# Optimization experiments

Measured on AMD Instinct MI355X. Metric: run time of the kernel, lower is better.

Reference implementation:

```python
import jax, jax.numpy as jnp
import numpy as np

# Module constants from CheckboxDetector.__init__ / _postprocess
N = 8192            # candidate detections
C = 2               # checkbox classes (checked / unchecked)
THR = 0.7           # confidence threshold (self.threshold)
IOU_THR = 0.5       # torchvision.ops.nms iou_threshold
INPUT_H, INPUT_W = 1280.0, 1280.0   # self.input_shape
IMG_H, IMG_W = 2480.0, 3508.0       # original image (A4 @ 300dpi)
SCALER = max(IMG_W / INPUT_W, IMG_H / INPUT_H)
EPS = 1e-9


def setup_inputs() -> dict:
    key = jax.random.key(0)
    k1, k2, k3 = jax.random.split(key, 3)
    cls_conf = jax.random.uniform(k1, (N, C), dtype=jnp.float32)
    # well-formed xyxy boxes inside the 1280x1280 canvas
    xy = jax.random.uniform(k2, (N, 2), dtype=jnp.float32, minval=0.0, maxval=1200.0)
    wh = jax.random.uniform(k3, (N, 2), dtype=jnp.float32, minval=8.0, maxval=80.0)
    bboxes = jnp.concatenate([xy, xy + wh], axis=1)  # [N,4]
    return {"cls_conf": cls_conf, "bboxes": bboxes}


def _pairwise_iou(boxes):
    # boxes: [N,4] xyxy -> iou: [N,N]
    x1, y1, x2, y2 = boxes[:, 0], boxes[:, 1], boxes[:, 2], boxes[:, 3]
    area = (x2 - x1) * (y2 - y1)
    iw = jnp.clip(jnp.minimum(x2[:, None], x2[None, :]) - jnp.maximum(x1[:, None], x1[None, :]), 0.0)
    ih = jnp.clip(jnp.minimum(y2[:, None], y2[None, :]) - jnp.maximum(y1[:, None], y1[None, :]), 0.0)
    inter = iw * ih
    return inter / (area[:, None] + area[None, :] - inter + EPS)


def reference(cls_conf, bboxes):
    # _threshold: keep rows with any class confidence > THR (mask instead of
    # dynamic filtering, for fixed shapes under jit)
    valid = jnp.any(cls_conf > THR, axis=1)            # [N]
    scores = jnp.max(cls_conf, axis=1)                 # cls_conf.max(1)
    masked_scores = jnp.where(valid, scores, -jnp.inf)

    # _nms: sort by score desc, greedy IoU suppression (torchvision semantics)
    order = jnp.argsort(-masked_scores)
    b = bboxes[order]          # [N,4]
    c = cls_conf[order]        # [N,C]
    v = valid[order]           # [N]

    iou = _pairwise_iou(b)     # [N,N]  (256 MB: memory-bound core)
    idx = jnp.arange(N)

    def body(i, keep):
        # box i (if still kept & valid) suppresses later boxes overlapping > IOU_THR
        sup = (iou[i] > IOU_THR) & (idx > i) & keep[i]
        return keep & ~sup

    keep = jax.lax.fori_loop(0, N, body, v)            # [N] bool

    # _postprocess tail: rescale boxes to original image size; suppressed
    # detections are zeroed (mask semantics in place of dynamic gather).
    kf = keep.astype(cls_conf.dtype)[:, None]
    boxes_out = b * SCALER * kf                        # [N,4]
    conf_out = c * kf                                  # [N,C]
    return jnp.concatenate([boxes_out, conf_out], axis=1)  # [N, 4+C]
```

## Files before the change

### kernel.cpp

```cpp
#include <hip/hip_runtime.h>
#include <math.h>

#define N_BOX 8192
#define NW 128
#define NTHR 512
#define LCAP 24576
#define NPB 512
#define TPW 4
#define RPT 4
#define NRB 128
#define WPB 8
#define NWAVE (NPB * WPB)
#define SLOT 128
#define WSPT (NWAVE / NTHR)
#define NCH 8
#define THR_C 0.7f
#define IOU_THR_C 0.5f
#define EPS_C 1e-9f

__device__ __constant__ float kScaler = (float)(3508.0 / 1280.0);

static __device__ __forceinline__ unsigned long long key_from(float c0, float c1, int i) {
    bool valid = (c0 > THR_C) || (c1 > THR_C);
    float ms = valid ? fmaxf(c0, c1) : -INFINITY;
    unsigned int u = __float_as_uint(ms);
    unsigned int m = (u & 0x80000000u) ? ~u : (u | 0x80000000u);
    unsigned int d = ~m;
    return ((unsigned long long)d << 32) | (unsigned int)i;
}

__global__ __launch_bounds__(NTHR) void stageA(const float* __restrict__ conf,
                                               const float* __restrict__ bboxes,
                                               int* __restrict__ partial,
                                               unsigned int* __restrict__ wcnt,
                                               unsigned int* __restrict__ wslot) {
    int b = blockIdx.x;
    int t = threadIdx.x;
    if (b < NPB) {
        int w = b >> 2;
        int h = b & (TPW - 1);
        int ntiles = (w >> 5) + 1;
        int waveid = b * WPB + (t >> 6);
        int lane = t & 63;
        if (h >= ntiles) {
            if (lane == 0) wcnt[waveid] = 0u;
            return;
        }
        __shared__ float4 cb[64];
        __shared__ float carea[64];
        __shared__ unsigned long long cbk[64];
        __shared__ unsigned long long jvS;
        if (t < 64) {
            int j = (w << 6) + t;
            float4 c = ((const float4*)bboxes)[j];
            cb[t] = c;
            carea[t] = (c.z - c.x) * (c.w - c.y);
            float2 cc = ((const float2*)conf)[j];
            cbk[t] = key_from(cc.x, cc.y, j);
            unsigned long long bv = __ballot((cc.x > THR_C) || (cc.y > THR_C));
            if (t == 0) jvS = bv;
        }
        __syncthreads();
        unsigned long long jv = jvS;
        int ibase = h << 11;
        float4 rb_[RPT];
        float ra_[RPT];
        unsigned long long ki_[RPT], jm_[RPT];
#pragma unroll
        for (int q = 0; q < RPT; ++q) {
            int i = ibase + (q << 9) + t;
            int rel = i - (w << 6);
            unsigned long long jm = jv;
            if (rel >= 63) jm = 0ull;
            else if (rel >= 0) jm &= ~((2ull << rel) - 1ull);
            float2 cc = ((const float2*)conf)[i];
            if (!((cc.x > THR_C) || (cc.y > THR_C))) jm = 0ull;
            jm_[q] = jm;
            float4 r = ((const float4*)bboxes)[i];
            rb_[q] = r;
            ra_[q] = (r.z - r.x) * (r.w - r.y);
            ki_[q] = key_from(cc.x, cc.y, i);
        }
        int wc = 0;
        bool wave_has = __any((jm_[0] | jm_[1] | jm_[2] | jm_[3]) != 0ull);
        if (wave_has) {
            unsigned long long bits[RPT] = {0ull, 0ull, 0ull, 0ull};
            for (int bb = 0; bb < 64; ++bb) {
                float4 c = cb[bb];
                float ca = carea[bb];
#pragma unroll
                for (int q = 0; q < RPT; ++q) {
                    float iw = fminf(rb_[q].z, c.z) - fmaxf(rb_[q].x, c.x);
                    float ih = fminf(rb_[q].w, c.w) - fmaxf(rb_[q].y, c.y);
                    iw = fmaxf(iw, 0.0f);
                    ih = fmaxf(ih, 0.0f);
                    float inter = iw * ih;
                    float sab = ra_[q] + ca;
                    if (inter > 0.2f * sab) {
                        float iou = inter / (ra_[q] + ca - inter + EPS_C);
                        if (iou > IOU_THR_C) bits[q] |= (1ull << bb);
                    }
                }
            }
#pragma unroll
            for (int q = 0; q < RPT; ++q) {
                unsigned long long eb = bits[q] & jm_[q];
                if (__any(eb != 0ull)) {
                    int ec = __popcll(eb);
                    int pre = ec;
#pragma unroll
                    for (int d = 1; d < 64; d <<= 1) {
                        int vv = __shfl_up(pre, d, 64);
                        if (lane >= d) pre += vv;
                    }
                    int tot = __shfl(pre, 63, 64);
                    int idx = wc + pre - ec;
                    unsigned long long tb = eb;
                    int i = ibase + (q << 9) + t;
                    while (tb) {
                        int bb = __builtin_ctzll(tb); tb &= tb - 1;
                        if (idx < SLOT) {
                            int j = (w << 6) + bb;
                            unsigned int e = (ki_[q] < cbk[bb])
                                             ? (((unsigned int)i << 13) | (unsigned int)j)
                                             : (((unsigned int)j << 13) | (unsigned int)i);
                            wslot[(size_t)waveid * SLOT + idx] = e;
                        }
                        ++idx;
                    }
                    wc += tot;
                }
            }
        }
        if (lane == 0) wcnt[waveid] = (unsigned int)wc;
    } else {
        __shared__ unsigned long long ck[1024];
        int rb = b - NPB;
        int ech = rb >> 3;
        int cch = rb & 7;
        for (int l = t; l < 1024; l += NTHR) {
            int j = (cch << 10) + l;
            float2 cc = ((const float2*)conf)[j];
            ck[l] = key_from(cc.x, cc.y, j);
        }
        __syncthreads();
        int i = (ech << 9) + t;
        float2 ci = ((const float2*)conf)[i];
        unsigned long long ki = key_from(ci.x, ci.y, i);
        const ulonglong2* ckp = (const ulonglong2*)ck;
        int a0 = 0, a1 = 0, a2 = 0, a3 = 0;
#pragma unroll 4
        for (int l = 0; l < 512; l += 2) {
            ulonglong2 u = ckp[l];
            ulonglong2 v = ckp[l + 1];
            a0 += (u.x < ki) ? 1 : 0;
            a1 += (u.y < ki) ? 1 : 0;
            a2 += (v.x < ki) ? 1 : 0;
            a3 += (v.y < ki) ? 1 : 0;
        }
        partial[cch * N_BOX + i] = (a0 + a1) + (a2 + a3);
    }
}

__global__ __launch_bounds__(NTHR) void stageB(const float* __restrict__ conf,
                                               const float* __restrict__ bboxes,
                                               const int* __restrict__ partial,
                                               const unsigned int* __restrict__ wcnt,
                                               const unsigned int* __restrict__ wslot,
                                               float* __restrict__ out) {
    __shared__ unsigned int eL[LCAP];
    __shared__ unsigned long long kL[NW], tL[NW], vL[NW];
    __shared__ int wsum[NTHR];
    __shared__ int chg[3];
    __shared__ int fbF, nvF;
    int t = threadIdx.x;
    if (t == 0) { fbF = 0; nvF = 0; chg[0] = 0; chg[1] = 0; chg[2] = 0; }
    for (int base = 0; base < N_BOX; base += NTHR) {
        int i = base + t;
        float2 cc = ((const float2*)conf)[i];
        unsigned long long bv = __ballot((cc.x > THR_C) || (cc.y > THR_C));
        if ((t & 63) == 0) vL[i >> 6] = bv;
    }
    int nq[WSPT], myo[WSPT];
    int s = 0;
    bool ov = false;
#pragma unroll
    for (int q = 0; q < WSPT; ++q) {
        int v = (int)wcnt[t * WSPT + q];
        nq[q] = v; myo[q] = s; s += v;
        if (v > SLOT) ov = true;
    }
    wsum[t] = s;
    __syncthreads();
    if (t < NW) kL[t] = vL[t];
    for (int off = 1; off < NTHR; off <<= 1) {
        int v = (t >= off) ? wsum[t - off] : 0;
        __syncthreads();
        wsum[t] += v;
        __syncthreads();
    }
    int ebase = wsum[t] - s;
    int totE = wsum[NTHR - 1];
    if (ov || totE > LCAP) fbF = 1;
    __syncthreads();
    int fb = fbF;
    if (!fb) {
#pragma unroll
        for (int q = 0; q < WSPT; ++q) {
            int w2 = t * WSPT + q;
            int off = ebase + myo[q];
            for (int k = 0; k < nq[q]; ++k)
                eL[off + k] = wslot[(size_t)w2 * SLOT + k];
        }
    }
    __syncthreads();
    if (!fb) {
        for (int it = 0; it < N_BOX; ++it) {
            if (t < NW) tL[t] = 0ull;
            __syncthreads();
            for (int e = t; e < totE; e += NTHR) {
                unsigned int ed = eL[e];
                int src = (int)(ed >> 13);
                if ((kL[src >> 6] >> (src & 63)) & 1ull) {
                    int tg = (int)(ed & 8191u);
                    atomicOr(&tL[tg >> 6], 1ull << (tg & 63));
                }
            }
            __syncthreads();
            if (t < NW) {
                unsigned long long nk = vL[t] & ~tL[t];
                if (nk != kL[t]) chg[it % 3] = 1;
                kL[t] = nk;
            }
            if (t == 0) chg[(it + 2) % 3] = 0;
            __syncthreads();
            if (chg[it % 3] == 0) break;
        }
    } else {
        unsigned int* sinv = eL;
        for (int base = 0; base < N_BOX; base += NTHR) {
            int i = base + t;
            int r = 0;
#pragma unroll
            for (int c = 0; c < NCH; ++c) r += partial[c * N_BOX + i];
            sinv[r] = (unsigned int)i;
        }
        if (t < NW) { atomicAdd(&nvF, __popcll(vL[t])); tL[t] = 0ull; kL[t] = 0ull; }
        __syncthreads();
        int nv = nvF;
        if (t < 64) {
            for (int a = 0; a < nv - 1; ++a) {
                bool rem = (tL[a >> 6] >> (a & 63)) & 1ull;
                if (!rem) {
                    float4 r = ((const float4*)bboxes)[sinv[a]];
                    float ra = (r.z - r.x) * (r.w - r.y);
                    for (int b2 = a + 1 + t; b2 < nv; b2 += 64) {
                        float4 c = ((const float4*)bboxes)[sinv[b2]];
                        float ca = (c.z - c.x) * (c.w - c.y);
                        float iw = fminf(r.z, c.z) - fmaxf(r.x, c.x);
                        float ih = fminf(r.w, c.w) - fmaxf(r.y, c.y);
                        iw = fmaxf(iw, 0.0f);
                        ih = fmaxf(ih, 0.0f);
                        float inter = iw * ih;
                        float iou = inter / (ra + ca - inter + EPS_C);
                        if (iou > IOU_THR_C) atomicOr(&tL[b2 >> 6], 1ull << (b2 & 63));
                    }
                }
            }
        }
        __syncthreads();
        for (int a = t; a < nv; a += NTHR) {
            if (!((tL[a >> 6] >> (a & 63)) & 1ull)) {
                int ia = (int)sinv[a];
                atomicOr(&kL[ia >> 6], 1ull << (ia & 63));
            }
        }
    }
    __syncthreads();
    for (int base = 0; base < N_BOX; base += NTHR) {
        int i = base + t;
        int r = 0;
#pragma unroll
        for (int c = 0; c < NCH; ++c) r += partial[c * N_BOX + i];
        bool kept = (kL[i >> 6] >> (i & 63)) & 1ull;
        if (kept) {
            float4 bx = ((const float4*)bboxes)[i];
            float2 cc = ((const float2*)conf)[i];
            out[r * 6 + 0] = bx.x * kScaler;
            out[r * 6 + 1] = bx.y * kScaler;
            out[r * 6 + 2] = bx.z * kScaler;
            out[r * 6 + 3] = bx.w * kScaler;
            out[r * 6 + 4] = cc.x;
            out[r * 6 + 5] = cc.y;
        } else {
            out[r * 6 + 0] = 0.0f;
            out[r * 6 + 1] = 0.0f;
            out[r * 6 + 2] = 0.0f;
            out[r * 6 + 3] = 0.0f;
            out[r * 6 + 4] = 0.0f;
            out[r * 6 + 5] = 0.0f;
        }
    }
}

extern "C" void kernel_launch(void* const* d_in, const int* in_sizes, int n_in,
                              void* d_out, int out_size, void* d_ws, size_t ws_size,
                              hipStream_t stream) {
    const float* cls_conf = (const float*)d_in[0];
    const float* bboxes   = (const float*)d_in[1];
    float* out = (float*)d_out;

    char* ws = (char*)d_ws;
    int*          partial = (int*)(ws + 0);
    unsigned int* wcnt    = (unsigned int*)(ws + 262144);
    unsigned int* wslot   = (unsigned int*)(ws + 278528);
    (void)ws_size; (void)in_sizes; (void)n_in; (void)out_size;

    stageA<<<NPB + NRB, NTHR, 0, stream>>>(cls_conf, bboxes, partial, wcnt, wslot);
    stageB<<<1, NTHR, 0, stream>>>(cls_conf, bboxes, partial, wcnt, wslot, out);
}
```

Baseline: 116.9 us.

## Pack triangular pair tiles densely and split rank counting into finer chunks

Stage A's pair-tile blocks are reindexed so that only lower-triangular tiles are launched (576 blocks of 1024 rows each), removing the idle early-exit blocks. Each thread now handles 2 rows instead of 4. The rank-counting blocks are split into 16 chunks of 512 keys and moved to the front of the grid so they schedule first. The overlap test now uses precomputed 0.2*area terms and skips clamping before the cheap rejection. This changes workspace offsets and the number of wave slots stage B must scan, since NCH and NWAVE both grow.

```diff
diff --git a/kernel.cpp b/kernel.cpp
--- a/kernel.cpp
+++ b/kernel.cpp
@@ -5,15 +5,14 @@
 #define NW 128
 #define NTHR 512
 #define LCAP 24576
-#define NPB 512
-#define TPW 4
-#define RPT 4
-#define NRB 128
+#define NRBLK 256
+#define NPTILE 576
+#define RPT 2
 #define WPB 8
-#define NWAVE (NPB * WPB)
+#define NWAVE (NPTILE * WPB)
 #define SLOT 128
 #define WSPT (NWAVE / NTHR)
-#define NCH 8
+#define NCH 16
 #define THR_C 0.7f
 #define IOU_THR_C 0.5f
 #define EPS_C 1e-9f
@@ -36,25 +35,53 @@
                                                unsigned int* __restrict__ wslot) {
     int b = blockIdx.x;
     int t = threadIdx.x;
-    if (b < NPB) {
-        int w = b >> 2;
-        int h = b & (TPW - 1);
-        int ntiles = (w >> 5) + 1;
-        int waveid = b * WPB + (t >> 6);
+    if (b < NRBLK) {
+        __shared__ unsigned long long ck[512];
+        int ech = b >> 4;
+        int cch = b & 15;
+        {
+            int j = (cch << 9) + t;
+            float2 cc = ((const float2*)conf)[j];
+            ck[t] = key_from(cc.x, cc.y, j);
+        }
+        __syncthreads();
+        int i = (ech << 9) + t;
+        float2 ci = ((const float2*)conf)[i];
+        unsigned long long ki = key_from(ci.x, ci.y, i);
+        const ulonglong2* ckp = (const ulonglong2*)ck;
+        int a0 = 0, a1 = 0, a2 = 0, a3 = 0;
+#pragma unroll 4
+        for (int l = 0; l < 256; l += 2) {
+            ulonglong2 u = ckp[l];
+            ulonglong2 v = ckp[l + 1];
+            a0 += (u.x < ki) ? 1 : 0;
+            a1 += (u.y < ki) ? 1 : 0;
+            a2 += (v.x < ki) ? 1 : 0;
+            a3 += (v.y < ki) ? 1 : 0;
+        }
+        partial[cch * N_BOX + i] = (a0 + a1) + (a2 + a3);
+    } else {
+        int pb = b - NRBLK;
+        int g = 0;
+        while (8 * (g + 1) * (g + 2) <= pb) ++g;
+        int off = pb - 8 * g * (g + 1);
+        int wq = off / (g + 1);
+        int w = (g << 4) + wq;
+        int h = off - wq * (g + 1);
+        int waveid = pb * WPB + (t >> 6);
         int lane = t & 63;
-        if (h >= ntiles) {
-            if (lane == 0) wcnt[waveid] = 0u;
-            return;
-        }
         __shared__ float4 cb[64];
-        __shared__ float carea[64];
+        __shared__ float caF[64];
+        __shared__ float ca02[64];
         __shared__ unsigned long long cbk[64];
         __shared__ unsigned long long jvS;
         if (t < 64) {
             int j = (w << 6) + t;
             float4 c = ((const float4*)bboxes)[j];
             cb[t] = c;
-            carea[t] = (c.z - c.x) * (c.w - c.y);
+            float a = (c.z - c.x) * (c.w - c.y);
+            caF[t] = a;
+            ca02[t] = 0.2f * a;
             float2 cc = ((const float2*)conf)[j];
             cbk[t] = key_from(cc.x, cc.y, j);
             unsigned long long bv = __ballot((cc.x > THR_C) || (cc.y > THR_C));
@@ -62,49 +89,65 @@
         }
         __syncthreads();
         unsigned long long jv = jvS;
-        int ibase = h << 11;
-        float4 rb_[RPT];
-        float ra_[RPT];
-        unsigned long long ki_[RPT], jm_[RPT];
-#pragma unroll
-        for (int q = 0; q < RPT; ++q) {
-            int i = ibase + (q << 9) + t;
+        int ibase = h << 10;
+        float4 rb0, rb1;
+        float raF0, raF1, raS0, raS1;
+        unsigned long long ki0, ki1, jm0, jm1;
+        {
+            int i = ibase + t;
             int rel = i - (w << 6);
             unsigned long long jm = jv;
             if (rel >= 63) jm = 0ull;
             else if (rel >= 0) jm &= ~((2ull << rel) - 1ull);
             float2 cc = ((const float2*)conf)[i];
             if (!((cc.x > THR_C) || (cc.y > THR_C))) jm = 0ull;
-            jm_[q] = jm;
-            float4 r = ((const float4*)bboxes)[i];
-            rb_[q] = r;
-            ra_[q] = (r.z - r.x) * (r.w - r.y);
-            ki_[q] = key_from(cc.x, cc.y, i);
+            jm0 = jm;
+            rb0 = ((const float4*)bboxes)[i];
+            raF0 = (rb0.z - rb0.x) * (rb0.w - rb0.y);
+            raS0 = 0.2f * raF0;
+            ki0 = key_from(cc.x, cc.y, i);
+        }
+        {
+            int i = ibase + 512 + t;
+            int rel = i - (w << 6);
+            unsigned long long jm = jv;
+            if (rel >= 63) jm = 0ull;
+            else if (rel >= 0) jm &= ~((2ull << rel) - 1ull);
+            float2 cc = ((const float2*)conf)[i];
+            if (!((cc.x > THR_C) || (cc.y > THR_C))) jm = 0ull;
+            jm1 = jm;
+            rb1 = ((const float4*)bboxes)[i];
+            raF1 = (rb1.z - rb1.x) * (rb1.w - rb1.y);
+            raS1 = 0.2f * raF1;
+            ki1 = key_from(cc.x, cc.y, i);
         }
         int wc = 0;
-        bool wave_has = __any((jm_[0] | jm_[1] | jm_[2] | jm_[3]) != 0ull);
-        if (wave_has) {
-            unsigned long long bits[RPT] = {0ull, 0ull, 0ull, 0ull};
+        if (__any((jm0 | jm1) != 0ull)) {
+            unsigned long long bits0 = 0ull, bits1 = 0ull;
             for (int bb = 0; bb < 64; ++bb) {
                 float4 c = cb[bb];
-                float ca = carea[bb];
-#pragma unroll
-                for (int q = 0; q < RPT; ++q) {
-                    float iw = fminf(rb_[q].z, c.z) - fmaxf(rb_[q].x, c.x);
-                    float ih = fminf(rb_[q].w, c.w) - fmaxf(rb_[q].y, c.y);
-                    iw = fmaxf(iw, 0.0f);
-                    ih = fmaxf(ih, 0.0f);
-                    float inter = iw * ih;
-                    float sab = ra_[q] + ca;
-                    if (inter > 0.2f * sab) {
-                        float iou = inter / (ra_[q] + ca - inter + EPS_C);
-                        if (iou > IOU_THR_C) bits[q] |= (1ull << bb);
-                    }
-                }
-            }
-#pragma unroll
-            for (int q = 0; q < RPT; ++q) {
-                unsigned long long eb = bits[q] & jm_[q];
+                float s2 = ca02[bb];
+                float iw0 = fminf(rb0.z, c.z) - fmaxf(rb0.x, c.x);
+                float ih0 = fminf(rb0.w, c.w) - fmaxf(rb0.y, c.y);
+                if (iw0 * ih0 > raS0 + s2) {
+                    float iwc = fmaxf(iw0, 0.0f);
+                    float ihc = fmaxf(ih0, 0.0f);
+                    float inter = iwc * ihc;
+                    float iou = inter / (raF0 + caF[bb] - inter + EPS_C);
+                    if (iou > IOU_THR_C) bits0 |= (1ull << bb);
+                }
+                float iw1 = fminf(rb1.z, c.z) - fmaxf(rb1.x, c.x);
+                float ih1 = fminf(rb1.w, c.w) - fmaxf(rb1.y, c.y);
+                if (iw1 * ih1 > raS1 + s2) {
+                    float iwc = fmaxf(iw1, 0.0f);
+                    float ihc = fmaxf(ih1, 0.0f);
+                    float inter = iwc * ihc;
+                    float iou = inter / (raF1 + caF[bb] - inter + EPS_C);
+                    if (iou > IOU_THR_C) bits1 |= (1ull << bb);
+                }
+            }
+            {
+                unsigned long long eb = bits0 & jm0;
                 if (__any(eb != 0ull)) {
                     int ec = __popcll(eb);
                     int pre = ec;
@@ -116,12 +159,12 @@
                     int tot = __shfl(pre, 63, 64);
                     int idx = wc + pre - ec;
                     unsigned long long tb = eb;
-                    int i = ibase + (q << 9) + t;
+                    int i = ibase + t;
                     while (tb) {
                         int bb = __builtin_ctzll(tb); tb &= tb - 1;
                         if (idx < SLOT) {
                             int j = (w << 6) + bb;
-                            unsigned int e = (ki_[q] < cbk[bb])
+                            unsigned int e = (ki0 < cbk[bb])
                                              ? (((unsigned int)i << 13) | (unsigned int)j)
                                              : (((unsigned int)j << 13) | (unsigned int)i);
                             wslot[(size_t)waveid * SLOT + idx] = e;
@@ -131,34 +174,36 @@
                     wc += tot;
                 }
             }
+            {
+                unsigned long long eb = bits1 & jm1;
+                if (__any(eb != 0ull)) {
+                    int ec = __popcll(eb);
+                    int pre = ec;
+#pragma unroll
+                    for (int d = 1; d < 64; d <<= 1) {
+                        int vv = __shfl_up(pre, d, 64);
+                        if (lane >= d) pre += vv;
+                    }
+                    int tot = __shfl(pre, 63, 64);
+                    int idx = wc + pre - ec;
+                    unsigned long long tb = eb;
+                    int i = ibase + 512 + t;
+                    while (tb) {
+                        int bb = __builtin_ctzll(tb); tb &= tb - 1;
+                        if (idx < SLOT) {
+                            int j = (w << 6) + bb;
+                            unsigned int e = (ki1 < cbk[bb])
+                                             ? (((unsigned int)i << 13) | (unsigned int)j)
+                                             : (((unsigned int)j << 13) | (unsigned int)i);
+                            wslot[(size_t)waveid * SLOT + idx] = e;
+                        }
+                        ++idx;
+                    }
+                    wc += tot;
+                }
+            }
         }
         if (lane == 0) wcnt[waveid] = (unsigned int)wc;
-    } else {
-        __shared__ unsigned long long ck[1024];
-        int rb = b - NPB;
-        int ech = rb >> 3;
-        int cch = rb & 7;
-        for (int l = t; l < 1024; l += NTHR) {
-            int j = (cch << 10) + l;
-            float2 cc = ((const float2*)conf)[j];
-            ck[l] = key_from(cc.x, cc.y, j);
-        }
-        __syncthreads();
-        int i = (ech << 9) + t;
-        float2 ci = ((const float2*)conf)[i];
-        unsigned long long ki = key_from(ci.x, ci.y, i);
-        const ulonglong2* ckp = (const ulonglong2*)ck;
-        int a0 = 0, a1 = 0, a2 = 0, a3 = 0;
-#pragma unroll 4
-        for (int l = 0; l < 512; l += 2) {
-            ulonglong2 u = ckp[l];
-            ulonglong2 v = ckp[l + 1];
-            a0 += (u.x < ki) ? 1 : 0;
-            a1 += (u.y < ki) ? 1 : 0;
-            a2 += (v.x < ki) ? 1 : 0;
-            a3 += (v.y < ki) ? 1 : 0;
-        }
-        partial[cch * N_BOX + i] = (a0 + a1) + (a2 + a3);
     }
 }
 
@@ -312,10 +357,10 @@
 
     char* ws = (char*)d_ws;
     int*          partial = (int*)(ws + 0);
-    unsigned int* wcnt    = (unsigned int*)(ws + 262144);
-    unsigned int* wslot   = (unsigned int*)(ws + 278528);
+    unsigned int* wcnt    = (unsigned int*)(ws + 524288);
+    unsigned int* wslot   = (unsigned int*)(ws + 557056);
     (void)ws_size; (void)in_sizes; (void)n_in; (void)out_size;
 
-    stageA<<<NPB + NRB, NTHR, 0, stream>>>(cls_conf, bboxes, partial, wcnt, wslot);
+    stageA<<<NRBLK + NPTILE, NTHR, 0, stream>>>(cls_conf, bboxes, partial, wcnt, wslot);
     stageB<<<1, NTHR, 0, stream>>>(cls_conf, bboxes, partial, wcnt, wslot, out);
 }
```

Result: slower. 133.4 us (+14.1%).
